# Kernel tuning notes

Measured on AMD Instinct MI355X. Metric: run time of the kernel, lower is better.

## Reference

```python
import jax, jax.numpy as jnp
import numpy as np

B = 262144
STEPS = 15            # Program.steps = var(15)
SPEED = 5.0           # Program.straight_speed
TRAJ_IDX = np.array([10, 1, 2, 3, 4, 5, 6, 7, 8, 17])
FEAT_IDX = np.array([1, 2, 3, 4, 9, 17])


def setup_inputs() -> dict:
    key = jax.random.key(0)
    ks = jax.random.split(key, 9)
    x = jax.random.normal(ks[0], (B, 18), dtype=jnp.float32)
    x = x.at[:, 0].set(0.0)  # loop counter i starts at 0 -> exactly 15 iterations
    return {
        "x": x,
        "c1w": jax.random.normal(ks[1], (2,), jnp.float32) * 0.5,
        "c1b": jax.random.normal(ks[2], (1,), jnp.float32) * 0.1,
        "c2w": jax.random.normal(ks[3], (2,), jnp.float32) * 0.5,
        "c2b": jax.random.normal(ks[4], (1,), jnp.float32) * 0.1,
        "l1w": jax.random.normal(ks[5], (4, 32), jnp.float32) * 0.3,
        "l1b": jax.random.normal(ks[6], (32,), jnp.float32) * 0.1,
        "l2w": jax.random.normal(ks[7], (32, 5), jnp.float32) * 0.3,
        "l2b": jax.random.normal(ks[8], (5,), jnp.float32) * 0.1,
    }


def _classifier(feat, c1w, c1b, c2w, c2b, l1w, l1b, l2w, l2b):
    # feat: [B,6] -> conv1d(k=2): [B,5] -> conv1d(k=2): [B,4] -> 32 -> 5, sigmoid
    h = jax.nn.relu(c1w[0] * feat[:, :-1] + c1w[1] * feat[:, 1:] + c1b)
    h = jax.nn.relu(c2w[0] * h[:, :-1] + c2w[1] * h[:, 1:] + c2b)
    h = jax.nn.relu(h @ l1w + l1b)
    return jax.nn.sigmoid(h @ l2w + l2b)  # [B,5]


def _distance(s):
    return (s[:, 1] - s[:, 3]) ** 2 + (s[:, 2] - s[:, 4]) ** 2


def _program(x, c1w, c1b, c2w, c2b, l1w, l1b, l2w, l2b):
    s = x.at[:, 10].set(_distance(x))          # initial assign_distance
    traj0 = s[:, TRAJ_IDX]                      # initial trajectory_update

    def step(s, _):
        # assign_branch_probability
        p = _classifier(s[:, FEAT_IDX], c1w, c1b, c2w, c2b, l1w, l1b, l2w, l2b)
        s = (s.at[:, 5].set(p[:, 0]).at[:, 6].set(p[:, 1]).at[:, 7].set(p[:, 2])
              .at[:, 8].set(p[:, 3]).at[:, 17].set(p[:, 4]))
        p5, p6, p7, p8 = p[:, 0], p[:, 1], p[:, 2], p[:, 3]
        # assign_comparison_block: pairwise diffs a..f at indices 11..16
        a, b, c = p6 - p5, p7 - p5, p8 - p5
        d, e, f = p7 - p6, p8 - p6, p8 - p7
        s = (s.at[:, 11].set(a).at[:, 12].set(b).at[:, 13].set(c)
              .at[:, 14].set(d).at[:, 15].set(e).at[:, 16].set(f))
        # ifelse_argmax_ITE: nested compare against comparison_bar=0.0
        dx_c = jnp.where(c <= 0.0, 0.0, SPEED);  st_c = jnp.where(c <= 0.0, 0.0, 3.0)   # cruise vs right
        dx_f = jnp.where(f <= 0.0, 0.0, SPEED);  st_f = jnp.where(f <= 0.0, 2.0, 3.0)   # straight vs right
        dx_e = jnp.where(e <= 0.0, -SPEED, SPEED); st_e = jnp.where(e <= 0.0, 1.0, 3.0)  # left vs right
        dx_b = jnp.where(b <= 0.0, dx_c, dx_f);  st_b = jnp.where(b <= 0.0, st_c, st_f)
        dx_d = jnp.where(d <= 0.0, dx_e, dx_f);  st_d = jnp.where(d <= 0.0, st_e, st_f)
        dx   = jnp.where(a <= 0.0, dx_b, dx_d);  st   = jnp.where(a <= 0.0, st_b, st_d)
        s = s.at[:, 1].add(dx).at[:, 9].set(st)
        # assign_y1, assign_x2, assign_update_i, assign_distance
        s = s.at[:, 2].add(SPEED).at[:, 3].add(SPEED).at[:, 0].add(1.0)
        s = s.at[:, 10].set(_distance(s))
        return s, s[:, TRAJ_IDX]

    s, recs = jax.lax.scan(step, s, None, length=STEPS)
    traj = jnp.concatenate([traj0[:, None, :], jnp.moveaxis(recs, 0, 1)], axis=1)  # [B,16,10]
    return jnp.concatenate([s, traj.reshape(s.shape[0], -1)], axis=1)  # [B, 18+160]


def reference(x, c1w, c1b, c2w, c2b, l1w, l1b, l2w, l2b):
    return _program(x, c1w, c1b, c2w, c2b, l1w, l1b, l2w, l2b)
```

## Files before the change

### kernel.cpp

```cpp
#include <hip/hip_runtime.h>


constexpr int kB     = 262144;
constexpr int kSteps = 15;
constexpr int PAD    = 33;

__device__ __forceinline__ float relu_(float v) { return fmaxf(v, 0.0f); }
__device__ __forceinline__ float sigmoid_(float v) {
    return __builtin_amdgcn_rcpf(1.0f + __expf(-v));
}

__global__ __launch_bounds__(256) void Program_4578435138231_kernel(
    const float* __restrict__ x,
    const float* __restrict__ c1w, const float* __restrict__ c1b,
    const float* __restrict__ c2w, const float* __restrict__ c2b,
    const float* __restrict__ l1w, const float* __restrict__ l1b,
    const float* __restrict__ l2w, const float* __restrict__ l2b,
    float* __restrict__ out)
{
    __shared__ float lds[256 * PAD];
    const int tid = threadIdx.x;
    const int R0  = blockIdx.x * 256;

    {
        const float* xblk = x + (size_t)R0 * 18;
        #pragma unroll
        for (int j = 0; j < 18; ++j) {
            int flat = tid + 256 * j;
            float v  = xblk[flat];
            int r = (int)(((unsigned)flat * 58255u) >> 20);
            int c = flat - r * 18;
            lds[r * PAD + c] = v;
        }
    }
    __syncthreads();
    float s[18];
    #pragma unroll
    for (int j = 0; j < 18; ++j) s[j] = lds[tid * PAD + j];
    __syncthreads();

    const float cw10 = c1w[0], cw11 = c1w[1], cb1 = c1b[0];
    const float cw20 = c2w[0], cw21 = c2w[1], cb2 = c2b[0];

    {
        float dA = s[1] - s[3], dB = s[2] - s[4];
        s[10] = dA * dA + dB * dB;
    }

    float* lr = lds + tid * PAD;

    auto flush32 = [&](int wcol) {
        __syncthreads();
        const int rr = tid >> 5, cc = tid & 31;
        const float* lp = lds + rr * PAD + cc;
        float*       op = out + (size_t)(R0 + rr) * 178 + wcol + cc;
        #pragma unroll
        for (int j = 0; j < 32; ++j) {
            op[(size_t)(8 * j) * 178] = lp[8 * j * PAD];
        }
        __syncthreads();
    };

    int wstart = 18;
    int nextb  = 50;

    lr[0] = s[10]; lr[1] = s[1];  lr[2] = s[2]; lr[3] = s[3]; lr[4] = s[4];
    lr[5] = s[5];  lr[6] = s[6];  lr[7] = s[7]; lr[8] = s[8]; lr[9] = s[17];

    #pragma unroll 1
    for (int t = 0; t < kSteps; ++t) {
        float f0 = s[1], f1 = s[2], f2 = s[3], f3 = s[4], f4 = s[9], f5 = s[17];
        float h10 = relu_(cw10 * f0 + cw11 * f1 + cb1);
        float h11 = relu_(cw10 * f1 + cw11 * f2 + cb1);
        float h12 = relu_(cw10 * f2 + cw11 * f3 + cb1);
        float h13 = relu_(cw10 * f3 + cw11 * f4 + cb1);
        float h14 = relu_(cw10 * f4 + cw11 * f5 + cb1);
        float g0 = relu_(cw20 * h10 + cw21 * h11 + cb2);
        float g1 = relu_(cw20 * h11 + cw21 * h12 + cb2);
        float g2 = relu_(cw20 * h12 + cw21 * h13 + cb2);
        float g3 = relu_(cw20 * h13 + cw21 * h14 + cb2);

        float p0 = l2b[0], p1 = l2b[1], p2 = l2b[2], p3 = l2b[3], p4 = l2b[4];
        #pragma unroll
        for (int k = 0; k < 32; ++k) {
            float h = g0 * l1w[k] + g1 * l1w[32 + k] + g2 * l1w[64 + k]
                    + g3 * l1w[96 + k] + l1b[k];
            h = relu_(h);
            p0 += h * l2w[5 * k + 0];
            p1 += h * l2w[5 * k + 1];
            p2 += h * l2w[5 * k + 2];
            p3 += h * l2w[5 * k + 3];
            p4 += h * l2w[5 * k + 4];
        }
        p0 = sigmoid_(p0); p1 = sigmoid_(p1); p2 = sigmoid_(p2);
        p3 = sigmoid_(p3); p4 = sigmoid_(p4);

        s[5] = p0; s[6] = p1; s[7] = p2; s[8] = p3; s[17] = p4;
        float a = p1 - p0, b = p2 - p0, c = p3 - p0;
        float d = p2 - p1, e = p3 - p1, f = p3 - p2;
        s[11] = a; s[12] = b; s[13] = c; s[14] = d; s[15] = e; s[16] = f;

        float dx_c = (c <= 0.f) ? 0.f  : 5.f,  st_c = (c <= 0.f) ? 0.f : 3.f;
        float dx_f = (f <= 0.f) ? 0.f  : 5.f,  st_f = (f <= 0.f) ? 2.f : 3.f;
        float dx_e = (e <= 0.f) ? -5.f : 5.f,  st_e = (e <= 0.f) ? 1.f : 3.f;
        float dx_b = (b <= 0.f) ? dx_c : dx_f, st_b = (b <= 0.f) ? st_c : st_f;
        float dx_d = (d <= 0.f) ? dx_e : dx_f, st_d = (d <= 0.f) ? st_e : st_f;
        float dx   = (a <= 0.f) ? dx_b : dx_d, st   = (a <= 0.f) ? st_b : st_d;

        s[1] += dx; s[9] = st;
        s[2] += 5.f; s[3] += 5.f; s[0] += 1.f;
        float dA = s[1] - s[3], dB = s[2] - s[4];
        s[10] = dA * dA + dB * dB;

        float v0 = s[10], v1 = s[1], v2 = s[2], v3 = s[3], v4 = s[4];
        float v5 = s[5],  v6 = s[6], v7 = s[7], v8 = s[8], v9 = s[17];
        const int c0 = 28 + 10 * t;
        const int kk = nextb - c0;
        int off = c0 - wstart;
        if (kk >= 10) {
            lr[off + 0] = v0; lr[off + 1] = v1; lr[off + 2] = v2;
            lr[off + 3] = v3; lr[off + 4] = v4; lr[off + 5] = v5;
            lr[off + 6] = v6; lr[off + 7] = v7; lr[off + 8] = v8;
            lr[off + 9] = v9;
            if (kk == 10) {
                flush32(wstart);
                wstart = nextb; nextb += 32;
            }
        } else {
            if (kk > 0) lr[off + 0] = v0;
            if (kk > 1) lr[off + 1] = v1;
            if (kk > 2) lr[off + 2] = v2;
            if (kk > 3) lr[off + 3] = v3;
            if (kk > 4) lr[off + 4] = v4;
            if (kk > 5) lr[off + 5] = v5;
            if (kk > 6) lr[off + 6] = v6;
            if (kk > 7) lr[off + 7] = v7;
            if (kk > 8) lr[off + 8] = v8;
            if (kk > 9) lr[off + 9] = v9;
            flush32(wstart);
            wstart = nextb; nextb += 32;
            off = c0 - wstart;
            if (kk <= 0) lr[off + 0] = v0;
            if (kk <= 1) lr[off + 1] = v1;
            if (kk <= 2) lr[off + 2] = v2;
            if (kk <= 3) lr[off + 3] = v3;
            if (kk <= 4) lr[off + 4] = v4;
            if (kk <= 5) lr[off + 5] = v5;
            if (kk <= 6) lr[off + 6] = v6;
            if (kk <= 7) lr[off + 7] = v7;
            if (kk <= 8) lr[off + 8] = v8;
            if (kk <= 9) lr[off + 9] = v9;
        }
    }

    __syncthreads();
    #pragma unroll
    for (int j = 0; j < 18; ++j) lr[j] = s[j];
    __syncthreads();
    #pragma unroll
    for (int j = 0; j < 18; ++j) {
        int flat = tid + 256 * j;
        int r = (int)(((unsigned)flat * 58255u) >> 20);
        int c = flat - r * 18;
        out[(size_t)(R0 + r) * 178 + c] = lds[r * PAD + c];
    }
}

extern "C" void kernel_launch(void* const* d_in, const int* in_sizes, int n_in,
                              void* d_out, int out_size, void* d_ws, size_t ws_size,
                              hipStream_t stream) {
    const float* x   = (const float*)d_in[0];
    const float* c1w = (const float*)d_in[1];
    const float* c1b = (const float*)d_in[2];
    const float* c2w = (const float*)d_in[3];
    const float* c2b = (const float*)d_in[4];
    const float* l1w = (const float*)d_in[5];
    const float* l1b = (const float*)d_in[6];
    const float* l2w = (const float*)d_in[7];
    const float* l2b = (const float*)d_in[8];
    float* out = (float*)d_out;

    Program_4578435138231_kernel<<<kB / 256, 256, 0, stream>>>(
        x, c1w, c1b, c2w, c2b, l1w, l1b, l2w, l2b, out);
}
```

Measured before the change: 285.3 us.

## Process two rows per thread with packed float2 FMA math

```diff
diff --git a/kernel.cpp b/kernel.cpp
--- a/kernel.cpp
+++ b/kernel.cpp
@@ -1,16 +1,29 @@
 #include <hip/hip_runtime.h>
 
+
+typedef float f32x2 __attribute__((ext_vector_type(2)));
 
 constexpr int kB     = 262144;
 constexpr int kSteps = 15;
 constexpr int PAD    = 33;
-
-__device__ __forceinline__ float relu_(float v) { return fmaxf(v, 0.0f); }
+constexpr int TPB    = 128;
+constexpr int RPB    = 256;
+
+__device__ __forceinline__ f32x2 splat(float v) { return (f32x2){v, v}; }
+__device__ __forceinline__ f32x2 fma2(f32x2 a, f32x2 b, f32x2 c) {
+    return __builtin_elementwise_fma(a, b, c);
+}
+__device__ __forceinline__ f32x2 relu2(f32x2 v) {
+    return __builtin_elementwise_max(v, splat(0.0f));
+}
 __device__ __forceinline__ float sigmoid_(float v) {
     return __builtin_amdgcn_rcpf(1.0f + __expf(-v));
 }
-
-__global__ __launch_bounds__(256) void Program_4578435138231_kernel(
+__device__ __forceinline__ f32x2 sigmoid2(f32x2 z) {
+    return (f32x2){sigmoid_(z.x), sigmoid_(z.y)};
+}
+
+__global__ __launch_bounds__(TPB) void Program_4578435138231_kernel(
     const float* __restrict__ x,
     const float* __restrict__ c1w, const float* __restrict__ c1b,
     const float* __restrict__ c2w, const float* __restrict__ c2b,
@@ -18,15 +31,15 @@
     const float* __restrict__ l2w, const float* __restrict__ l2b,
     float* __restrict__ out)
 {
-    __shared__ float lds[256 * PAD];
+    __shared__ float lds[RPB * PAD];
     const int tid = threadIdx.x;
-    const int R0  = blockIdx.x * 256;
+    const int R0  = blockIdx.x * RPB;
 
     {
         const float* xblk = x + (size_t)R0 * 18;
         #pragma unroll
-        for (int j = 0; j < 18; ++j) {
-            int flat = tid + 256 * j;
+        for (int j = 0; j < 36; ++j) {
+            int flat = tid + TPB * j;
             float v  = xblk[flat];
             int r = (int)(((unsigned)flat * 58255u) >> 20);
             int c = flat - r * 18;
@@ -34,20 +47,23 @@
         }
     }
     __syncthreads();
-    float s[18];
+    f32x2 s[18];
     #pragma unroll
-    for (int j = 0; j < 18; ++j) s[j] = lds[tid * PAD + j];
+    for (int j = 0; j < 18; ++j)
+        s[j] = (f32x2){lds[tid * PAD + j], lds[(tid + TPB) * PAD + j]};
     __syncthreads();
 
     const float cw10 = c1w[0], cw11 = c1w[1], cb1 = c1b[0];
     const float cw20 = c2w[0], cw21 = c2w[1], cb2 = c2b[0];
-
-    {
-        float dA = s[1] - s[3], dB = s[2] - s[4];
-        s[10] = dA * dA + dB * dB;
-    }
-
-    float* lr = lds + tid * PAD;
+    const float b20 = l2b[0], b21 = l2b[1], b22 = l2b[2], b23 = l2b[3], b24 = l2b[4];
+    const f32x2 W10 = splat(cw10), W11 = splat(cw11), B1 = splat(cb1);
+    const f32x2 W20 = splat(cw20), W21 = splat(cw21), B2 = splat(cb2);
+
+    { f32x2 dA = s[1] - s[3], dB = s[2] - s[4]; s[10] = fma2(dA, dA, dB * dB); }
+
+    float* lrA = lds + tid * PAD;
+    float* lrB = lds + (tid + TPB) * PAD;
+    auto rec = [&](int idx, f32x2 v) { lrA[idx] = v.x; lrB[idx] = v.y; };
 
     auto flush32 = [&](int wcol) {
         __syncthreads();
@@ -55,8 +71,8 @@
         const float* lp = lds + rr * PAD + cc;
         float*       op = out + (size_t)(R0 + rr) * 178 + wcol + cc;
         #pragma unroll
-        for (int j = 0; j < 32; ++j) {
-            op[(size_t)(8 * j) * 178] = lp[8 * j * PAD];
+        for (int j = 0; j < 64; ++j) {
+            op[(size_t)(4 * j) * 178] = lp[4 * j * PAD];
         }
         __syncthreads();
     };
@@ -64,102 +80,112 @@
     int wstart = 18;
     int nextb  = 50;
 
-    lr[0] = s[10]; lr[1] = s[1];  lr[2] = s[2]; lr[3] = s[3]; lr[4] = s[4];
-    lr[5] = s[5];  lr[6] = s[6];  lr[7] = s[7]; lr[8] = s[8]; lr[9] = s[17];
+    rec(0, s[10]); rec(1, s[1]); rec(2, s[2]); rec(3, s[3]); rec(4, s[4]);
+    rec(5, s[5]);  rec(6, s[6]); rec(7, s[7]); rec(8, s[8]); rec(9, s[17]);
 
     #pragma unroll 1
     for (int t = 0; t < kSteps; ++t) {
-        float f0 = s[1], f1 = s[2], f2 = s[3], f3 = s[4], f4 = s[9], f5 = s[17];
-        float h10 = relu_(cw10 * f0 + cw11 * f1 + cb1);
-        float h11 = relu_(cw10 * f1 + cw11 * f2 + cb1);
-        float h12 = relu_(cw10 * f2 + cw11 * f3 + cb1);
-        float h13 = relu_(cw10 * f3 + cw11 * f4 + cb1);
-        float h14 = relu_(cw10 * f4 + cw11 * f5 + cb1);
-        float g0 = relu_(cw20 * h10 + cw21 * h11 + cb2);
-        float g1 = relu_(cw20 * h11 + cw21 * h12 + cb2);
-        float g2 = relu_(cw20 * h12 + cw21 * h13 + cb2);
-        float g3 = relu_(cw20 * h13 + cw21 * h14 + cb2);
-
-        float p0 = l2b[0], p1 = l2b[1], p2 = l2b[2], p3 = l2b[3], p4 = l2b[4];
+        f32x2 f0 = s[1], f1 = s[2], f2 = s[3], f3 = s[4], f4 = s[9], f5 = s[17];
+        f32x2 h10 = relu2(fma2(W10, f0, fma2(W11, f1, B1)));
+        f32x2 h11 = relu2(fma2(W10, f1, fma2(W11, f2, B1)));
+        f32x2 h12 = relu2(fma2(W10, f2, fma2(W11, f3, B1)));
+        f32x2 h13 = relu2(fma2(W10, f3, fma2(W11, f4, B1)));
+        f32x2 h14 = relu2(fma2(W10, f4, fma2(W11, f5, B1)));
+        f32x2 g0 = relu2(fma2(W20, h10, fma2(W21, h11, B2)));
+        f32x2 g1 = relu2(fma2(W20, h11, fma2(W21, h12, B2)));
+        f32x2 g2 = relu2(fma2(W20, h12, fma2(W21, h13, B2)));
+        f32x2 g3 = relu2(fma2(W20, h13, fma2(W21, h14, B2)));
+
+        f32x2 p0 = splat(b20), p1 = splat(b21), p2 = splat(b22);
+        f32x2 p3 = splat(b23), p4 = splat(b24);
         #pragma unroll
         for (int k = 0; k < 32; ++k) {
-            float h = g0 * l1w[k] + g1 * l1w[32 + k] + g2 * l1w[64 + k]
-                    + g3 * l1w[96 + k] + l1b[k];
-            h = relu_(h);
-            p0 += h * l2w[5 * k + 0];
-            p1 += h * l2w[5 * k + 1];
-            p2 += h * l2w[5 * k + 2];
-            p3 += h * l2w[5 * k + 3];
-            p4 += h * l2w[5 * k + 4];
-        }
-        p0 = sigmoid_(p0); p1 = sigmoid_(p1); p2 = sigmoid_(p2);
-        p3 = sigmoid_(p3); p4 = sigmoid_(p4);
+            f32x2 h = fma2(splat(l1w[k]),      g0,
+                      fma2(splat(l1w[32 + k]), g1,
+                      fma2(splat(l1w[64 + k]), g2,
+                      fma2(splat(l1w[96 + k]), g3, splat(l1b[k])))));
+            h = relu2(h);
+            p0 = fma2(h, splat(l2w[5 * k + 0]), p0);
+            p1 = fma2(h, splat(l2w[5 * k + 1]), p1);
+            p2 = fma2(h, splat(l2w[5 * k + 2]), p2);
+            p3 = fma2(h, splat(l2w[5 * k + 3]), p3);
+            p4 = fma2(h, splat(l2w[5 * k + 4]), p4);
+        }
+        p0 = sigmoid2(p0); p1 = sigmoid2(p1); p2 = sigmoid2(p2);
+        p3 = sigmoid2(p3); p4 = sigmoid2(p4);
 
         s[5] = p0; s[6] = p1; s[7] = p2; s[8] = p3; s[17] = p4;
-        float a = p1 - p0, b = p2 - p0, c = p3 - p0;
-        float d = p2 - p1, e = p3 - p1, f = p3 - p2;
-        s[11] = a; s[12] = b; s[13] = c; s[14] = d; s[15] = e; s[16] = f;
-
-        float dx_c = (c <= 0.f) ? 0.f  : 5.f,  st_c = (c <= 0.f) ? 0.f : 3.f;
-        float dx_f = (f <= 0.f) ? 0.f  : 5.f,  st_f = (f <= 0.f) ? 2.f : 3.f;
-        float dx_e = (e <= 0.f) ? -5.f : 5.f,  st_e = (e <= 0.f) ? 1.f : 3.f;
-        float dx_b = (b <= 0.f) ? dx_c : dx_f, st_b = (b <= 0.f) ? st_c : st_f;
-        float dx_d = (d <= 0.f) ? dx_e : dx_f, st_d = (d <= 0.f) ? st_e : st_f;
-        float dx   = (a <= 0.f) ? dx_b : dx_d, st   = (a <= 0.f) ? st_b : st_d;
-
-        s[1] += dx; s[9] = st;
-        s[2] += 5.f; s[3] += 5.f; s[0] += 1.f;
-        float dA = s[1] - s[3], dB = s[2] - s[4];
-        s[10] = dA * dA + dB * dB;
-
-        float v0 = s[10], v1 = s[1], v2 = s[2], v3 = s[3], v4 = s[4];
-        float v5 = s[5],  v6 = s[6], v7 = s[7], v8 = s[8], v9 = s[17];
+        f32x2 a2 = p1 - p0, b2 = p2 - p0, c2 = p3 - p0;
+        f32x2 d2 = p2 - p1, e2 = p3 - p1, q2 = p3 - p2;
+        s[11] = a2; s[12] = b2; s[13] = c2; s[14] = d2; s[15] = e2; s[16] = q2;
+
+        auto move = [](float a, float b, float c, float d, float e, float f,
+                       float& dx, float& st) {
+            float dx_c = (c <= 0.f) ? 0.f  : 5.f,  st_c = (c <= 0.f) ? 0.f : 3.f;
+            float dx_f = (f <= 0.f) ? 0.f  : 5.f,  st_f = (f <= 0.f) ? 2.f : 3.f;
+            float dx_e = (e <= 0.f) ? -5.f : 5.f,  st_e = (e <= 0.f) ? 1.f : 3.f;
+            float dx_b = (b <= 0.f) ? dx_c : dx_f, st_b = (b <= 0.f) ? st_c : st_f;
+            float dx_d = (d <= 0.f) ? dx_e : dx_f, st_d = (d <= 0.f) ? st_e : st_f;
+            dx = (a <= 0.f) ? dx_b : dx_d;
+            st = (a <= 0.f) ? st_b : st_d;
+        };
+        float dxA, stA, dxB, stB;
+        move(a2.x, b2.x, c2.x, d2.x, e2.x, q2.x, dxA, stA);
+        move(a2.y, b2.y, c2.y, d2.y, e2.y, q2.y, dxB, stB);
+
+        s[1] += (f32x2){dxA, dxB};
+        s[9]  = (f32x2){stA, stB};
+        s[2] += splat(5.f); s[3] += splat(5.f); s[0] += splat(1.f);
+        { f32x2 dA = s[1] - s[3], dB = s[2] - s[4]; s[10] = fma2(dA, dA, dB * dB); }
+
+        f32x2 v0 = s[10], v1 = s[1], v2 = s[2], v3 = s[3], v4 = s[4];
+        f32x2 v5 = s[5],  v6 = s[6], v7 = s[7], v8 = s[8], v9 = s[17];
         const int c0 = 28 + 10 * t;
         const int kk = nextb - c0;
         int off = c0 - wstart;
         if (kk >= 10) {
-            lr[off + 0] = v0; lr[off + 1] = v1; lr[off + 2] = v2;
-            lr[off + 3] = v3; lr[off + 4] = v4; lr[off + 5] = v5;
-            lr[off + 6] = v6; lr[off + 7] = v7; lr[off + 8] = v8;
-            lr[off + 9] = v9;
+            rec(off + 0, v0); rec(off + 1, v1); rec(off + 2, v2);
+            rec(off + 3, v3); rec(off + 4, v4); rec(off + 5, v5);
+            rec(off + 6, v6); rec(off + 7, v7); rec(off + 8, v8);
+            rec(off + 9, v9);
             if (kk == 10) {
                 flush32(wstart);
                 wstart = nextb; nextb += 32;
             }
         } else {
-            if (kk > 0) lr[off + 0] = v0;
-            if (kk > 1) lr[off + 1] = v1;
-            if (kk > 2) lr[off + 2] = v2;
-            if (kk > 3) lr[off + 3] = v3;
-            if (kk > 4) lr[off + 4] = v4;
-            if (kk > 5) lr[off + 5] = v5;
-            if (kk > 6) lr[off + 6] = v6;
-            if (kk > 7) lr[off + 7] = v7;
-            if (kk > 8) lr[off + 8] = v8;
-            if (kk > 9) lr[off + 9] = v9;
+            if (kk > 0) rec(off + 0, v0);
+            if (kk > 1) rec(off + 1, v1);
+            if (kk > 2) rec(off + 2, v2);
+            if (kk > 3) rec(off + 3, v3);
+            if (kk > 4) rec(off + 4, v4);
+            if (kk > 5) rec(off + 5, v5);
+            if (kk > 6) rec(off + 6, v6);
+            if (kk > 7) rec(off + 7, v7);
+            if (kk > 8) rec(off + 8, v8);
+            if (kk > 9) rec(off + 9, v9);
             flush32(wstart);
             wstart = nextb; nextb += 32;
             off = c0 - wstart;
-            if (kk <= 0) lr[off + 0] = v0;
-            if (kk <= 1) lr[off + 1] = v1;
-            if (kk <= 2) lr[off + 2] = v2;
-            if (kk <= 3) lr[off + 3] = v3;
-            if (kk <= 4) lr[off + 4] = v4;
-            if (kk <= 5) lr[off + 5] = v5;
-            if (kk <= 6) lr[off + 6] = v6;
-            if (kk <= 7) lr[off + 7] = v7;
-            if (kk <= 8) lr[off + 8] = v8;
-            if (kk <= 9) lr[off + 9] = v9;
+            if (kk <= 0) rec(off + 0, v0);
+            if (kk <= 1) rec(off + 1, v1);
+            if (kk <= 2) rec(off + 2, v2);
+            if (kk <= 3) rec(off + 3, v3);
+            if (kk <= 4) rec(off + 4, v4);
+            if (kk <= 5) rec(off + 5, v5);
+            if (kk <= 6) rec(off + 6, v6);
+            if (kk <= 7) rec(off + 7, v7);
+            if (kk <= 8) rec(off + 8, v8);
+            if (kk <= 9) rec(off + 9, v9);
         }
     }
 
     __syncthreads();
     #pragma unroll
-    for (int j = 0; j < 18; ++j) lr[j] = s[j];
+    for (int j = 0; j < 18; ++j) { lrA[j] = s[j].x; lrB[j] = s[j].y; }
     __syncthreads();
     #pragma unroll
-    for (int j = 0; j < 18; ++j) {
-        int flat = tid + 256 * j;
+    for (int j = 0; j < 36; ++j) {
+        int flat = tid + TPB * j;
         int r = (int)(((unsigned)flat * 58255u) >> 20);
         int c = flat - r * 18;
         out[(size_t)(R0 + r) * 178 + c] = lds[r * PAD + c];
@@ -180,6 +206,6 @@
     const float* l2b = (const float*)d_in[8];
     float* out = (float*)d_out;
 
-    Program_4578435138231_kernel<<<kB / 256, 256, 0, stream>>>(
+    Program_4578435138231_kernel<<<kB / RPB, TPB, 0, stream>>>(
         x, c1w, c1b, c2w, c2b, l1w, l1b, l2w, l2b, out);
 }
```

Measured after the change: 286.2 us. About the same (+0.3%).
